# Kernel optimization log

Hardware: AMD Instinct MI355X
Metric: run time of the kernel (lower is better)

Reference implementation:

```python
import jax, jax.numpy as jnp
import numpy as np

HIDDEN = 128
N_NODES = 50000
N_EDGES = 640000


def setup_inputs() -> dict:
    key = jax.random.key(0)
    k1, k2, k3, k4, k5, k6, k7 = jax.random.split(key, 7)
    z = jax.random.normal(k1, (N_NODES, HIDDEN), dtype=jnp.float32)
    edge_index = jax.random.randint(k2, (2, N_EDGES), 0, N_NODES, dtype=jnp.int64)
    # Linear params (torch default uniform(-1/sqrt(fan_in), 1/sqrt(fan_in)))
    b1 = 1.0 / np.sqrt(2 * HIDDEN)
    W1 = jax.random.uniform(k3, (HIDDEN, 2 * HIDDEN), jnp.float32, -b1, b1)
    bias1 = jax.random.uniform(k4, (HIDDEN,), jnp.float32, -b1, b1)
    b2 = 1.0 / np.sqrt(HIDDEN)
    W2 = jax.random.uniform(k5, (1, HIDDEN), jnp.float32, -b2, b2)
    bias2 = jax.random.uniform(k6, (1,), jnp.float32, -b2, b2)
    return {"z": z, "W1": W1, "bias1": bias1, "W2": W2, "bias2": bias2,
            "edge_index": edge_index}


def reference(z, W1, bias1, W2, bias2, edge_index):
    # Gather endpoint embeddings: [E, H] each
    z_src = z[edge_index[0]]
    z_dst = z[edge_index[1]]
    h = jnp.concatenate([z_src, z_dst], axis=-1)  # [E, 2H]
    h = jax.nn.relu(h @ W1.T + bias1)             # [E, H]
    out = h @ W2.T + bias2                        # [E, 1]
    return out.reshape(-1)
```

## Files before the change

### kernel.cpp

```cpp
#include <hip/hip_runtime.h>
#include <hip/hip_bf16.h>


#define N_NODES 50000
#define N_EDGES 640000
#define H 128

using bf16 = __hip_bfloat16;
typedef __attribute__((ext_vector_type(8))) short short8;
typedef __attribute__((ext_vector_type(4))) float f32x4;

#define GLD_LDS16(g, l)                                                     \
  __builtin_amdgcn_global_load_lds(                                         \
      (const __attribute__((address_space(1))) void*)(g),                   \
      (__attribute__((address_space(3))) void*)(l), 16, 0, 0)

static __device__ __forceinline__ short bfbits(float x) {
  __hip_bfloat16 h = __float2bfloat16(x);
  return *reinterpret_cast<short*>(&h);
}

static __device__ __forceinline__ short8 pack8(float4 a, float4 b) {
  short8 r;
  r[0] = bfbits(a.x); r[1] = bfbits(a.y); r[2] = bfbits(a.z); r[3] = bfbits(a.w);
  r[4] = bfbits(b.x); r[5] = bfbits(b.y); r[6] = bfbits(b.z); r[7] = bfbits(b.w);
  return r;
}

__global__ __launch_bounds__(256) void w_to_bf16(const float* __restrict__ W1,
                                                 bf16* __restrict__ Wb) {
  const int u = blockIdx.x * 256 + threadIdx.x;
  const int o = u >> 4, k8 = (u & 15) * 8;
  const float4* src = reinterpret_cast<const float4*>(
      W1 + (size_t)(o & (H - 1)) * (2 * H) + (o >> 7) * H + k8);
  *reinterpret_cast<short8*>(Wb + (size_t)o * H + k8) = pack8(src[0], src[1]);
}

#define HP 136

__global__ __launch_bounds__(256) void precompute_uv(
    const float* __restrict__ z, const bf16* __restrict__ Wb,
    bf16* __restrict__ U, bf16* __restrict__ V) {
  __shared__ float ldsF[32 * H];
  __shared__ bf16 ldsH[32 * HP];
  const int tid = threadIdx.x;
  const int lane = tid & 63;
  const int s = tid >> 6;
  const int l15 = lane & 15, quad = lane >> 4;
  const int nodebase = blockIdx.x * 32;

  {
    int r0 = nodebase + s * 8;
    if (r0 > N_NODES - 8) r0 = N_NODES - 8;
    const float* gsrc = z + (size_t)r0 * H + lane * 4;
    float* ldst = ldsF + s * 8 * H;
#pragma unroll
    for (int j = 0; j < 4; ++j) GLD_LDS16(gsrc + j * 256, ldst + j * 256);
  }

  short8 wf[4][4];
#pragma unroll
  for (int t = 0; t < 4; ++t) {
    const bf16* wp = Wb + (size_t)(s * 64 + t * 16 + l15) * H + quad * 8;
#pragma unroll
    for (int q = 0; q < 4; ++q)
      wf[t][q] = *reinterpret_cast<const short8*>(wp + q * 32);
  }

  __syncthreads();

  {
    const int row = tid >> 3, off = (tid & 7) * 16;
    const float4* fp = reinterpret_cast<const float4*>(ldsF + row * H + off);
    const float4 a = fp[0], b = fp[1], c = fp[2], d = fp[3];
    *reinterpret_cast<short8*>(&ldsH[row * HP + off]) = pack8(a, b);
    *reinterpret_cast<short8*>(&ldsH[row * HP + off + 8]) = pack8(c, d);
  }
  __syncthreads();

  short8 zf[2][4];
#pragma unroll
  for (int m = 0; m < 2; ++m)
#pragma unroll
    for (int q = 0; q < 4; ++q)
      zf[m][q] = *reinterpret_cast<const short8*>(
          &ldsH[(m * 16 + l15) * HP + quad * 8 + q * 32]);

  f32x4 acc[2][4] = {};
#pragma unroll
  for (int m = 0; m < 2; ++m)
#pragma unroll
    for (int t = 0; t < 4; ++t)
#pragma unroll
      for (int q = 0; q < 4; ++q)
        acc[m][t] =
            __builtin_amdgcn_mfma_f32_16x16x32_bf16(wf[t][q], zf[m][q], acc[m][t], 0, 0, 0);

  bf16* epi = reinterpret_cast<bf16*>(ldsF);
#pragma unroll
  for (int m = 0; m < 2; ++m) {
    const int nl = m * 16 + l15;
#pragma unroll
    for (int t = 0; t < 4; ++t) {
      const int o = s * 64 + t * 16 + quad * 4;
      ushort4 st;
      st.x = (unsigned short)bfbits(acc[m][t][0]);
      st.y = (unsigned short)bfbits(acc[m][t][1]);
      st.z = (unsigned short)bfbits(acc[m][t][2]);
      st.w = (unsigned short)bfbits(acc[m][t][3]);
      *reinterpret_cast<ushort4*>(epi + nl * 256 + o) = st;
    }
  }
  __syncthreads();

#pragma unroll
  for (int half = 0; half < 2; ++half) {
    bf16* base = half ? V : U;
#pragma unroll
    for (int it = 0; it < 2; ++it) {
      const int nl = s * 8 + it * 4 + (lane >> 4);
      const int oc = (lane & 15) * 8;
      const short8 v = *reinterpret_cast<const short8*>(epi + nl * 256 + half * H + oc);
      const int n = nodebase + nl;
      if (n < N_NODES)
        *reinterpret_cast<short8*>(base + (size_t)n * H + oc) = v;
    }
  }
}

static __device__ __forceinline__ void acc2(unsigned u, unsigned v,
                                            float b1lo, float b1hi,
                                            float w2lo, float w2hi, float& sum) {
  const float ulo = __uint_as_float(u << 16);
  const float uhi = __uint_as_float(u & 0xffff0000u);
  const float vlo = __uint_as_float(v << 16);
  const float vhi = __uint_as_float(v & 0xffff0000u);
  float h0 = ulo + vlo + b1lo; h0 = fmaxf(h0, 0.f);
  float h1 = uhi + vhi + b1hi; h1 = fmaxf(h1, 0.f);
  sum = fmaf(h0, w2lo, sum);
  sum = fmaf(h1, w2hi, sum);
}

__global__ __launch_bounds__(256, 4) void edge_decode(
    const int* __restrict__ eidx, const bf16* __restrict__ Ub,
    const bf16* __restrict__ Vb, const float* __restrict__ bias1,
    const float* __restrict__ W2, const float* __restrict__ bias2,
    float* __restrict__ out) {
  const int lane = threadIdx.x & 63;
  const int w = blockIdx.x * 4 + (int)(threadIdx.x >> 6);
  const int chunk = w * 64;
  const int e8 = lane & 7;

  float b1r[16], w2r[16];
  const float4* bp = reinterpret_cast<const float4*>(bias1 + e8 * 16);
  const float4* wp = reinterpret_cast<const float4*>(W2 + e8 * 16);
#pragma unroll
  for (int q = 0; q < 4; ++q) {
    const float4 b = bp[q], wv = wp[q];
    b1r[q * 4 + 0] = b.x; b1r[q * 4 + 1] = b.y; b1r[q * 4 + 2] = b.z; b1r[q * 4 + 3] = b.w;
    w2r[q * 4 + 0] = wv.x; w2r[q * 4 + 1] = wv.y; w2r[q * 4 + 2] = wv.z; w2r[q * 4 + 3] = wv.w;
  }
  const float b2 = bias2[0];

  const int src = eidx[chunk + lane];
  const int dst = eidx[N_EDGES + chunk + lane];
  const uint4* U4 = reinterpret_cast<const uint4*>(Ub);
  const uint4* V4 = reinterpret_cast<const uint4*>(Vb);

  float res = 0.f;
#pragma unroll
  for (int half = 0; half < 2; ++half) {
    uint4 ua[4], ub[4], va[4], vb[4];
#pragma unroll
    for (int j = 0; j < 4; ++j) {
      const int i = half * 4 + j;
      const int sl = (lane & 56) + i;
      const int s_i = __shfl(src, sl);
      const int d_i = __shfl(dst, sl);
      const uint4* up = U4 + (size_t)s_i * 16 + e8 * 2;
      const uint4* vp = V4 + (size_t)d_i * 16 + e8 * 2;
      ua[j] = up[0]; ub[j] = up[1];
      va[j] = vp[0]; vb[j] = vp[1];
    }
#pragma unroll
    for (int j = 0; j < 4; ++j) {
      const int i = half * 4 + j;
      float sum = 0.f;
      acc2(ua[j].x, va[j].x, b1r[0],  b1r[1],  w2r[0],  w2r[1],  sum);
      acc2(ua[j].y, va[j].y, b1r[2],  b1r[3],  w2r[2],  w2r[3],  sum);
      acc2(ua[j].z, va[j].z, b1r[4],  b1r[5],  w2r[4],  w2r[5],  sum);
      acc2(ua[j].w, va[j].w, b1r[6],  b1r[7],  w2r[6],  w2r[7],  sum);
      acc2(ub[j].x, vb[j].x, b1r[8],  b1r[9],  w2r[8],  w2r[9],  sum);
      acc2(ub[j].y, vb[j].y, b1r[10], b1r[11], w2r[10], w2r[11], sum);
      acc2(ub[j].z, vb[j].z, b1r[12], b1r[13], w2r[12], w2r[13], sum);
      acc2(ub[j].w, vb[j].w, b1r[14], b1r[15], w2r[14], w2r[15], sum);
      sum += __shfl_xor(sum, 1);
      sum += __shfl_xor(sum, 2);
      sum += __shfl_xor(sum, 4);
      if (e8 == i) res = sum + b2;
    }
  }
  out[chunk + lane] = res;
}

extern "C" void kernel_launch(void* const* d_in, const int* in_sizes, int n_in,
                              void* d_out, int out_size, void* d_ws, size_t ws_size,
                              hipStream_t stream) {
  const float* z     = (const float*)d_in[0];
  const float* W1    = (const float*)d_in[1];
  const float* bias1 = (const float*)d_in[2];
  const float* W2    = (const float*)d_in[3];
  const float* bias2 = (const float*)d_in[4];
  const int*   eidx  = (const int*)d_in[5];
  float* out = (float*)d_out;

  bf16* U  = (bf16*)d_ws;
  bf16* V  = U + (size_t)N_NODES * H;
  bf16* Wb = V + (size_t)N_NODES * H;

  hipLaunchKernelGGL(w_to_bf16, dim3(16), dim3(256), 0, stream, W1, Wb);
  hipLaunchKernelGGL(precompute_uv, dim3((N_NODES + 31) / 32), dim3(256), 0, stream,
                     z, Wb, U, V);
  hipLaunchKernelGGL(edge_decode, dim3(N_EDGES / 64 / 4), dim3(256), 0, stream,
                     eidx, U, V, bias1, W2, bias2, out);
}
```

Measured before the change: 136.6 us.

## Fold bias1 into U/V precompute and make edge decode a persistent grid-stride kernel

Adds half of bias1 to both U and V in the precompute epilogue, so the edge kernel no longer loads bias registers or adds the bias per element. The edge kernel becomes a grid-stride loop over 1024 blocks instead of one wave per 64-edge chunk. A sched_barrier is placed between the gather loads and the compute to keep the loads issued together. Splitting the bias across two bf16-rounded values adds a small extra rounding error, and the fixed grid size may leave some compute units less occupied.

After: 139.1 us. No clear change (+1.8%).

```diff
diff --git a/kernel.cpp b/kernel.cpp
--- a/kernel.cpp
+++ b/kernel.cpp
@@ -40,7 +40,8 @@
 
 __global__ __launch_bounds__(256) void precompute_uv(
     const float* __restrict__ z, const bf16* __restrict__ Wb,
-    bf16* __restrict__ U, bf16* __restrict__ V) {
+    const float* __restrict__ bias1, bf16* __restrict__ U,
+    bf16* __restrict__ V) {
   __shared__ float ldsF[32 * H];
   __shared__ bf16 ldsH[32 * HP];
   const int tid = threadIdx.x;
@@ -103,11 +104,12 @@
 #pragma unroll
     for (int t = 0; t < 4; ++t) {
       const int o = s * 64 + t * 16 + quad * 4;
+      const float4 bv = *reinterpret_cast<const float4*>(bias1 + (o & (H - 1)));
       ushort4 st;
-      st.x = (unsigned short)bfbits(acc[m][t][0]);
-      st.y = (unsigned short)bfbits(acc[m][t][1]);
-      st.z = (unsigned short)bfbits(acc[m][t][2]);
-      st.w = (unsigned short)bfbits(acc[m][t][3]);
+      st.x = (unsigned short)bfbits(acc[m][t][0] + 0.5f * bv.x);
+      st.y = (unsigned short)bfbits(acc[m][t][1] + 0.5f * bv.y);
+      st.z = (unsigned short)bfbits(acc[m][t][2] + 0.5f * bv.z);
+      st.w = (unsigned short)bfbits(acc[m][t][3] + 0.5f * bv.w);
       *reinterpret_cast<ushort4*>(epi + nl * 256 + o) = st;
     }
   }
@@ -129,78 +131,79 @@
 }
 
 static __device__ __forceinline__ void acc2(unsigned u, unsigned v,
-                                            float b1lo, float b1hi,
                                             float w2lo, float w2hi, float& sum) {
   const float ulo = __uint_as_float(u << 16);
   const float uhi = __uint_as_float(u & 0xffff0000u);
   const float vlo = __uint_as_float(v << 16);
   const float vhi = __uint_as_float(v & 0xffff0000u);
-  float h0 = ulo + vlo + b1lo; h0 = fmaxf(h0, 0.f);
-  float h1 = uhi + vhi + b1hi; h1 = fmaxf(h1, 0.f);
+  float h0 = fmaxf(ulo + vlo, 0.f);
+  float h1 = fmaxf(uhi + vhi, 0.f);
   sum = fmaf(h0, w2lo, sum);
   sum = fmaf(h1, w2hi, sum);
 }
 
 __global__ __launch_bounds__(256, 4) void edge_decode(
     const int* __restrict__ eidx, const bf16* __restrict__ Ub,
-    const bf16* __restrict__ Vb, const float* __restrict__ bias1,
-    const float* __restrict__ W2, const float* __restrict__ bias2,
-    float* __restrict__ out) {
+    const bf16* __restrict__ Vb, const float* __restrict__ W2,
+    const float* __restrict__ bias2, float* __restrict__ out) {
   const int lane = threadIdx.x & 63;
-  const int w = blockIdx.x * 4 + (int)(threadIdx.x >> 6);
-  const int chunk = w * 64;
   const int e8 = lane & 7;
 
-  float b1r[16], w2r[16];
-  const float4* bp = reinterpret_cast<const float4*>(bias1 + e8 * 16);
+  float w2r[16];
   const float4* wp = reinterpret_cast<const float4*>(W2 + e8 * 16);
 #pragma unroll
   for (int q = 0; q < 4; ++q) {
-    const float4 b = bp[q], wv = wp[q];
-    b1r[q * 4 + 0] = b.x; b1r[q * 4 + 1] = b.y; b1r[q * 4 + 2] = b.z; b1r[q * 4 + 3] = b.w;
-    w2r[q * 4 + 0] = wv.x; w2r[q * 4 + 1] = wv.y; w2r[q * 4 + 2] = wv.z; w2r[q * 4 + 3] = wv.w;
+    const float4 wv = wp[q];
+    w2r[q * 4 + 0] = wv.x; w2r[q * 4 + 1] = wv.y;
+    w2r[q * 4 + 2] = wv.z; w2r[q * 4 + 3] = wv.w;
   }
   const float b2 = bias2[0];
 
-  const int src = eidx[chunk + lane];
-  const int dst = eidx[N_EDGES + chunk + lane];
   const uint4* U4 = reinterpret_cast<const uint4*>(Ub);
   const uint4* V4 = reinterpret_cast<const uint4*>(Vb);
 
-  float res = 0.f;
-#pragma unroll
-  for (int half = 0; half < 2; ++half) {
-    uint4 ua[4], ub[4], va[4], vb[4];
-#pragma unroll
-    for (int j = 0; j < 4; ++j) {
-      const int i = half * 4 + j;
-      const int sl = (lane & 56) + i;
-      const int s_i = __shfl(src, sl);
-      const int d_i = __shfl(dst, sl);
-      const uint4* up = U4 + (size_t)s_i * 16 + e8 * 2;
-      const uint4* vp = V4 + (size_t)d_i * 16 + e8 * 2;
-      ua[j] = up[0]; ub[j] = up[1];
-      va[j] = vp[0]; vb[j] = vp[1];
+  const int wid0 = blockIdx.x * 4 + (int)(threadIdx.x >> 6);
+  for (int c = wid0; c < N_EDGES / 64; c += 4096) {
+    const int chunk = c * 64;
+    const int src = eidx[chunk + lane];
+    const int dst = eidx[N_EDGES + chunk + lane];
+
+    float res = 0.f;
+#pragma unroll
+    for (int half = 0; half < 2; ++half) {
+      uint4 ua[4], ub[4], va[4], vb[4];
+#pragma unroll
+      for (int j = 0; j < 4; ++j) {
+        const int i = half * 4 + j;
+        const int sl = (lane & 56) | i;
+        const int s_i = __shfl(src, sl);
+        const int d_i = __shfl(dst, sl);
+        const uint4* up = U4 + (size_t)s_i * 16 + e8 * 2;
+        const uint4* vp = V4 + (size_t)d_i * 16 + e8 * 2;
+        ua[j] = up[0]; ub[j] = up[1];
+        va[j] = vp[0]; vb[j] = vp[1];
+      }
+      __builtin_amdgcn_sched_barrier(0);
+#pragma unroll
+      for (int j = 0; j < 4; ++j) {
+        const int i = half * 4 + j;
+        float sum = 0.f;
+        acc2(ua[j].x, va[j].x, w2r[0],  w2r[1],  sum);
+        acc2(ua[j].y, va[j].y, w2r[2],  w2r[3],  sum);
+        acc2(ua[j].z, va[j].z, w2r[4],  w2r[5],  sum);
+        acc2(ua[j].w, va[j].w, w2r[6],  w2r[7],  sum);
+        acc2(ub[j].x, vb[j].x, w2r[8],  w2r[9],  sum);
+        acc2(ub[j].y, vb[j].y, w2r[10], w2r[11], sum);
+        acc2(ub[j].z, vb[j].z, w2r[12], w2r[13], sum);
+        acc2(ub[j].w, vb[j].w, w2r[14], w2r[15], sum);
+        sum += __shfl_xor(sum, 1);
+        sum += __shfl_xor(sum, 2);
+        sum += __shfl_xor(sum, 4);
+        if (e8 == i) res = sum + b2;
+      }
     }
-#pragma unroll
-    for (int j = 0; j < 4; ++j) {
-      const int i = half * 4 + j;
-      float sum = 0.f;
-      acc2(ua[j].x, va[j].x, b1r[0],  b1r[1],  w2r[0],  w2r[1],  sum);
-      acc2(ua[j].y, va[j].y, b1r[2],  b1r[3],  w2r[2],  w2r[3],  sum);
-      acc2(ua[j].z, va[j].z, b1r[4],  b1r[5],  w2r[4],  w2r[5],  sum);
-      acc2(ua[j].w, va[j].w, b1r[6],  b1r[7],  w2r[6],  w2r[7],  sum);
-      acc2(ub[j].x, vb[j].x, b1r[8],  b1r[9],  w2r[8],  w2r[9],  sum);
-      acc2(ub[j].y, vb[j].y, b1r[10], b1r[11], w2r[10], w2r[11], sum);
-      acc2(ub[j].z, vb[j].z, b1r[12], b1r[13], w2r[12], w2r[13], sum);
-      acc2(ub[j].w, vb[j].w, b1r[14], b1r[15], w2r[14], w2r[15], sum);
-      sum += __shfl_xor(sum, 1);
-      sum += __shfl_xor(sum, 2);
-      sum += __shfl_xor(sum, 4);
-      if (e8 == i) res = sum + b2;
-    }
-  }
-  out[chunk + lane] = res;
+    out[chunk + lane] = res;
+  }
 }
 
 extern "C" void kernel_launch(void* const* d_in, const int* in_sizes, int n_in,
@@ -219,8 +222,8 @@
   bf16* Wb = V + (size_t)N_NODES * H;
 
   hipLaunchKernelGGL(w_to_bf16, dim3(16), dim3(256), 0, stream, W1, Wb);
-  hipLaunchKernelGGL(precompute_uv, dim3((N_NODES + 31) / 32), dim3(256), 0, stream,
-                     z, Wb, U, V);
-  hipLaunchKernelGGL(edge_decode, dim3(N_EDGES / 64 / 4), dim3(256), 0, stream,
-                     eidx, U, V, bias1, W2, bias2, out);
-}
+  hipLaunchKernelGGL(precompute_uv, dim3((N_NODES + 31) / 32), dim3(256), 0,
+                     stream, z, Wb, bias1, U, V);
+  hipLaunchKernelGGL(edge_decode, dim3(1024), dim3(256), 0, stream,
+                     eidx, U, V, W2, bias2, out);
+}
```
